# Performance work log

Measured on AMD Instinct MI355X. Metric: run time of the kernel, lower is better.

The kernel has to match this reference:

```python
import jax, jax.numpy as jnp
import numpy as np

B, S, E, H, L, A, OBS = 4, 1024, 512, 8, 4, 8, 128
D_HEAD = E // H
EPS = 1e-6
DECAY_SCALING = 1.0


def rmsnorm(x, scale):
    return x * jax.lax.rsqrt(jnp.mean(x * x, -1, keepdims=True) + EPS) * scale


def swiglu_ffn(x, w_gate, w_lin, w_out):
    return (jax.nn.silu(x @ w_gate) * (x @ w_lin)) @ w_out


def retention(x, h, logk, w_q, w_k, w_v, w_g, w_o, gns, gnb, ts, seg):
    # x:[B,S,E]  h:[B,H,d,d]  ts/seg:[B,S] int  logk:[H]
    q = (x @ w_q).reshape(B, S, H, D_HEAD).transpose(0, 2, 1, 3)
    k = (x @ w_k).reshape(B, S, H, D_HEAD).transpose(0, 2, 1, 3) / jnp.sqrt(jnp.asarray(D_HEAD, x.dtype))
    v = (x @ w_v).reshape(B, S, H, D_HEAD).transpose(0, 2, 1, 3)
    dt = (ts[:, :, None] - ts[:, None, :]).astype(x.dtype)            # [B,S,S]
    mask = (dt >= 0) & (seg[:, :, None] == seg[:, None, :])           # timestep-causal, same episode
    dt = jnp.where(mask, dt, 0.0)
    Dm = jnp.where(mask[:, None], jnp.exp(dt[:, None] * logk[None, :, None, None]), 0.0)  # [B,H,S,S]
    scores = jnp.einsum('bhnd,bhmd->bhnm', q, k) * Dm
    inner = jnp.einsum('bhnm,bhme->bhne', scores, v)
    tsf = ts.astype(x.dtype)
    fresh = (seg == 0).astype(x.dtype)                                # prev-chunk state only valid pre-done
    xi = jnp.exp((tsf + 1.0)[:, None, :] * logk[None, :, None]) * fresh[:, None, :]  # [B,H,S]
    cross = jnp.einsum('bhn,bhnd,bhde->bhne', xi, q, h)
    ret = inner + cross                                               # [B,H,S,d]
    # chunk-final recurrent state
    tmax = tsf[:, -1]
    eta = jnp.exp((tmax[:, None] - tsf)[:, None, :] * logk[None, :, None])
    eta = eta * (seg == seg[:, -1:]).astype(x.dtype)[:, None, :]
    keep = (seg[:, -1] == 0).astype(x.dtype)
    h_decay = jnp.exp((tmax + 1.0)[:, None] * logk[None, :]) * keep[:, None]  # [B,H]
    h_new = h * h_decay[..., None, None] + jnp.einsum('bhm,bhmd,bhme->bhde', eta, k, v)
    # per-head group norm (num_groups = n_head)
    y = ret.transpose(0, 2, 1, 3)                                     # [B,S,H,d]
    mu = jnp.mean(y, -1, keepdims=True)
    var = jnp.mean((y - mu) ** 2, -1, keepdims=True)
    y = ((y - mu) * jax.lax.rsqrt(var + EPS)).reshape(B, S, E) * gns + gnb
    out = (jax.nn.silu(x @ w_g) * y) @ w_o
    return out, h_new


def forward(obs, hstate, dones, timestep_id, ln_enc_scale, w_enc, ln_shared,
            wq, wk, wv, wg, wo, gn_scale, gn_bias, ln1_s, ln2_s,
            sw_gate, sw_lin, sw_out, head_w1, head_b1, head_ln, head_w2, head_b2):
    kappas = (1.0 - jnp.exp(jnp.linspace(jnp.log(1.0 / 32.0), jnp.log(1.0 / 512.0), H))) * DECAY_SCALING
    logk = jnp.log(kappas).astype(obs.dtype)
    seg = jnp.cumsum(dones, axis=-1)
    x = jax.nn.gelu(rmsnorm(obs, ln_enc_scale) @ w_enc)               # obs encoder
    new_h = jnp.zeros_like(hstate)
    for i in range(L):
        xin = rmsnorm(x, ln_shared)
        ret, hn = retention(xin, hstate[:, :, i], logk, wq[i], wk[i], wv[i], wg[i], wo[i],
                            gn_scale[i], gn_bias[i], timestep_id, seg)
        x1 = rmsnorm(xin + ret, ln1_s[i])
        x = rmsnorm(x1 + swiglu_ffn(x1, sw_gate[i], sw_lin[i], sw_out[i]), ln2_s[i])
        new_h = new_h.at[:, :, i].set(hn)
    z = jax.nn.gelu(x @ head_w1 + head_b1)
    v_loc = rmsnorm(z, head_ln) @ head_w2 + head_b2
    return v_loc, x, new_h


def setup_inputs() -> dict:
    key = jax.random.key(0)
    ks = jax.random.split(key, 16)
    sc = 0.02
    f = jnp.float32
    return {
        'obs': jax.random.normal(ks[0], (B, S, OBS), f),
        'hstate': jax.random.normal(ks[1], (B, H, L, D_HEAD, D_HEAD), f) * 0.1,
        'dones': (jax.random.uniform(ks[2], (B, S)) < 0.01).astype(jnp.int32),
        'timestep_id': jnp.broadcast_to(jnp.repeat(jnp.arange(S // A, dtype=jnp.int32), A)[None], (B, S)),
        'ln_enc_scale': jnp.ones((OBS,), f),
        'w_enc': jax.random.normal(ks[3], (OBS, E), f) * sc,
        'ln_shared': jnp.ones((E,), f),
        'wq': jax.random.normal(ks[4], (L, E, E), f) * sc,
        'wk': jax.random.normal(ks[5], (L, E, E), f) * sc,
        'wv': jax.random.normal(ks[6], (L, E, E), f) * sc,
        'wg': jax.random.normal(ks[7], (L, E, E), f) * sc,
        'wo': jax.random.normal(ks[8], (L, E, E), f) * sc,
        'gn_scale': jnp.ones((L, E), f),
        'gn_bias': jnp.zeros((L, E), f),
        'ln1_s': jnp.ones((L, E), f),
        'ln2_s': jnp.ones((L, E), f),
        'sw_gate': jax.random.normal(ks[9], (L, E, E), f) * sc,
        'sw_lin': jax.random.normal(ks[10], (L, E, E), f) * sc,
        'sw_out': jax.random.normal(ks[11], (L, E, E), f) * sc,
        'head_w1': jax.random.normal(ks[12], (E, E), f) * sc,
        'head_b1': jnp.zeros((E,), f),
        'head_ln': jnp.ones((E,), f),
        'head_w2': jax.random.normal(ks[13], (E, 1), f) * 0.01,
        'head_b2': jnp.zeros((1,), f),
    }


def reference(obs, hstate, dones, timestep_id, ln_enc_scale, w_enc, ln_shared,
              wq, wk, wv, wg, wo, gn_scale, gn_bias, ln1_s, ln2_s,
              sw_gate, sw_lin, sw_out, head_w1, head_b1, head_ln, head_w2, head_b2):
    return forward(obs, hstate, dones, timestep_id, ln_enc_scale, w_enc, ln_shared,
                   wq, wk, wv, wg, wo, gn_scale, gn_bias, ln1_s, ln2_s,
                   sw_gate, sw_lin, sw_out, head_w1, head_b1, head_ln, head_w2, head_b2)
```

## Files before the change

### kernel.cpp

```cpp
#include <hip/hip_runtime.h>
#include <math.h>

#define BN 4
#define SN 1024
#define EN 512
#define HN 8
#define LN 4
#define DN 64
#define OBSN 128
#define NR (BN*SN)
#define NB (NR*EN)
#define EPSF 1e-6f

typedef __attribute__((ext_vector_type(8))) short short8v;
typedef __attribute__((ext_vector_type(4))) float f32x4;
typedef unsigned short u16;

__device__ __forceinline__ float logk_of(int h){
    const float start = -3.4657359027997265f;
    const float step  = -0.3960841031771117f;
    return logf(1.0f - expf(start + step*(float)h));
}
__device__ __forceinline__ float geluf(float x){
    float x3 = x*x*x;
    return 0.5f*x*(1.0f + tanhf(0.7978845608028654f*(x + 0.044715f*x3)));
}
__device__ __forceinline__ float siluf(float x){
    return x / (1.0f + expf(-x));
}
__device__ __forceinline__ u16 f2bf(float x){
    union { float f; unsigned u; } v; v.f = x;
    unsigned r = v.u + 0x7FFFu + ((v.u >> 16) & 1u);
    return (u16)(r >> 16);
}
__device__ __forceinline__ float bf2f(u16 x){
    union { unsigned u; float f; } v; v.u = ((unsigned)x)<<16;
    return v.f;
}
__device__ __forceinline__ void load_lds16(const void* g, void* l){
    __builtin_amdgcn_global_load_lds((const __attribute__((address_space(1))) void*)g,
                                     (__attribute__((address_space(3))) void*)l, 16, 0, 0);
}
__device__ __forceinline__ int swz(int r, int bo){ return r*128 + (bo ^ ((r&7)<<4)); }

__device__ __forceinline__ float rx_of(int mode, const float* ssA, const float* ssB, int row){
    float rn = rsqrtf(ssA[row]*(1.f/512.f) + EPSF);
    if (mode==0) return rn;
    return rn*rsqrtf(rn*rn*ssB[row]*(1.f/512.f) + EPSF);
}

__global__ void seg_kernel(const int* __restrict__ dones, int* __restrict__ seg){
    __shared__ int sm[SN];
    int b = blockIdx.x, t = threadIdx.x;
    sm[t] = dones[b*SN + t];
    __syncthreads();
    for (int off=1; off<SN; off<<=1){
        int v = (t>=off) ? sm[t-off] : 0;
        __syncthreads();
        sm[t] += v;
        __syncthreads();
    }
    seg[b*SN + t] = sm[t];
}

__global__ void lnvq_kernel(const float* __restrict__ lnsh, const float* __restrict__ ln2,
                            float* __restrict__ lnvq){
    int k = threadIdx.x;
    #pragma unroll
    for (int l=0;l<LN;l++)
        lnvq[l*EN + k] = lnsh[k] * (l ? ln2[(l-1)*EN + k] : 1.f);
}

__global__ void wconv8_kernel(const float* w0, const float* w1, const float* w2,
                              const float* w3, const float* w4, const float* w5,
                              const float* w6, const float* w7,
                              const float* __restrict__ lnvq, const float* __restrict__ ln1,
                              u16* __restrict__ dst){
    __shared__ u16 tile[32][33];
    int z = blockIdx.z;
    int type = z>>2, layer = z&3;
    const float* srcs[8] = {w0,w1,w2,w3,w4,w5,w6,w7};
    const float* s = srcs[type] + (size_t)layer*EN*EN;
    u16* d = dst + ((size_t)type*LN + layer)*EN*EN;
    int k0 = blockIdx.y*32, m0 = blockIdx.x*32;
    int tx = threadIdx.x, ty = threadIdx.y;
    #pragma unroll
    for (int i=0;i<32;i+=8){
        int k = k0+ty+i;
        float sc = 1.f;
        if (type<4) sc = lnvq[layer*EN + k];
        else if (type==5 || type==6) sc = ln1[layer*EN + k];
        tile[tx][ty+i] = f2bf(s[(size_t)k*EN + m0+tx]*sc);
    }
    __syncthreads();
    #pragma unroll
    for (int i=0;i<32;i+=8)
        d[(size_t)(m0+ty+i)*EN + k0+tx] = tile[ty+i][tx];
}
__global__ void wconv_kernel(const float* __restrict__ src, u16* __restrict__ dst,
                             int K, int M){
    __shared__ u16 tile[32][33];
    int k0 = blockIdx.y*32, m0 = blockIdx.x*32;
    int tx = threadIdx.x, ty = threadIdx.y;
    #pragma unroll
    for (int i=0;i<32;i+=8)
        tile[tx][ty+i] = f2bf(src[(size_t)(k0+ty+i)*M + m0+tx]);
    __syncthreads();
    #pragma unroll
    for (int i=0;i<32;i+=8)
        dst[(size_t)(m0+ty+i)*K + k0+tx] = tile[ty+i][tx];
}

__global__ void rmsobs_kernel(const float* __restrict__ A, const float* __restrict__ scale,
                              u16* __restrict__ Ob){
    int row  = blockIdx.x*4 + (threadIdx.x>>6);
    int lane = threadIdx.x & 63;
    const float* a = A + (size_t)row*OBSN;
    float v0 = a[lane], v1 = a[lane+64];
    float ss = v0*v0 + v1*v1;
    #pragma unroll
    for (int off=32; off>0; off>>=1) ss += __shfl_xor(ss, off, 64);
    float rs = rsqrtf(ss*(1.0f/OBSN) + EPSF);
    Ob[(size_t)row*OBSN + lane]      = f2bf(v0*rs*scale[lane]);
    Ob[(size_t)row*OBSN + lane + 64] = f2bf(v1*rs*scale[lane+64]);
}

__device__ __forceinline__ void stage_tile(const u16* __restrict__ G, size_t rowBase,
                                           int K, int k0, u16* dst, int t){
    #pragma unroll
    for (int i=0;i<2;i++){
        int o = i*4096 + t*16;
        int grow = o>>7, gcolb = o&127;
        load_lds16(G + (rowBase+grow)*K + k0 + (gcolb>>1), (char*)dst + o);
    }
}
__device__ __forceinline__ void mma_tile(const u16* As, const u16* Bs, f32x4 acc[2][2],
                                         int wr, int wc, int lane){
    #pragma unroll
    for (int kk=0; kk<64; kk+=32){
        int kb = kk + (lane>>4)*8;
        short8v a[2], b[2];
        #pragma unroll
        for (int m=0;m<2;m++)
            a[m] = *(const short8v*)((const char*)As + (wr*32+m*16+(lane&15))*128 + kb*2);
        #pragma unroll
        for (int n=0;n<2;n++)
            b[n] = *(const short8v*)((const char*)Bs + (wc*32+n*16+(lane&15))*128 + kb*2);
        #pragma unroll
        for (int m=0;m<2;m++)
            #pragma unroll
            for (int n=0;n<2;n++)
                acc[m][n] = __builtin_amdgcn_mfma_f32_16x16x32_bf16(a[m], b[n], acc[m][n], 0,0,0);
    }
}
#define ZERO_ACC(acc) { _Pragma("unroll") for (int m=0;m<2;m++) _Pragma("unroll") for (int n=0;n<2;n++){ acc[m][n][0]=0.f;acc[m][n][1]=0.f;acc[m][n][2]=0.f;acc[m][n][3]=0.f; } }

__device__ __forceinline__ void ss_atomic(float v, float* __restrict__ ss, int row, int lane){
    #pragma unroll
    for (int off=1; off<16; off<<=1) v += __shfl_xor(v, off, 16);
    if ((lane&15)==0) atomicAdd(&ss[row], v);
}

__global__ __launch_bounds__(256) void gemm_enc(
    const u16* __restrict__ A, const u16* __restrict__ Wt,
    float* __restrict__ Xf, u16* __restrict__ Xb, float* __restrict__ ssA)
{
    __shared__ u16 As[2][64*64];
    __shared__ u16 Bs[2][64*64];
    int t = threadIdx.x;
    int row0 = blockIdx.y*64, col0 = blockIdx.x*64;
    int w = t>>6, lane = t&63;
    int wr = w>>1, wc = w&1;
    f32x4 acc[2][2];
    ZERO_ACC(acc);
    stage_tile(A, (size_t)row0, OBSN, 0, As[0], t);
    stage_tile(Wt, (size_t)col0, OBSN, 0, Bs[0], t);
    __syncthreads();
    for (int ti=0; ti<OBSN/64; ++ti){
        int cur = ti&1;
        if (ti+1 < OBSN/64){
            stage_tile(A, (size_t)row0, OBSN, (ti+1)*64, As[cur^1], t);
            stage_tile(Wt, (size_t)col0, OBSN, (ti+1)*64, Bs[cur^1], t);
        }
        mma_tile(As[cur], Bs[cur], acc, wr, wc, lane);
        __syncthreads();
    }
    #pragma unroll
    for (int m=0;m<2;m++){
        #pragma unroll
        for (int j=0;j<4;j++){
            int row = row0 + wr*32 + m*16 + (lane>>4)*4 + j;
            float sv = 0.f;
            #pragma unroll
            for (int n=0;n<2;n++){
                int col = col0 + wc*32 + n*16 + (lane&15);
                float x = geluf(acc[m][n][j]);
                Xf[(size_t)row*EN + col] = x;
                Xb[(size_t)row*EN + col] = f2bf(x);
                sv += x*x;
            }
            ss_atomic(sv, ssA, row, lane);
        }
    }
}

__global__ __launch_bounds__(256) void gemm_qkvg(
    const u16* __restrict__ A,
    const u16* __restrict__ WQ, const u16* __restrict__ WK,
    const u16* __restrict__ WV, const u16* __restrict__ WG,
    const float* __restrict__ ssA, const float* __restrict__ ssB, int mode,
    u16* __restrict__ Qbb, u16* __restrict__ Kbb,
    u16* __restrict__ VtT, u16* __restrict__ KtT, float* __restrict__ Gb)
{
    __shared__ u16 As[2][64*64];
    __shared__ u16 Bs[2][4][64*64];
    int t = threadIdx.x;
    int row0 = blockIdx.y*64, col0 = blockIdx.x*64;
    int w = t>>6, lane = t&63;
    int wr = w>>1, wc = w&1;
    f32x4 accQ[2][2], accK[2][2], accV[2][2], accG[2][2];
    ZERO_ACC(accQ); ZERO_ACC(accK); ZERO_ACC(accV); ZERO_ACC(accG);
    const u16* Ws[4] = {WQ, WK, WV, WG};

    stage_tile(A, (size_t)row0, EN, 0, As[0], t);
    #pragma unroll
    for (int wt=0; wt<4; wt++) stage_tile(Ws[wt], (size_t)col0, EN, 0, Bs[0][wt], t);
    __syncthreads();
    for (int ti=0; ti<EN/64; ++ti){
        int cur = ti&1;
        if (ti+1 < EN/64){
            stage_tile(A, (size_t)row0, EN, (ti+1)*64, As[cur^1], t);
            #pragma unroll
            for (int wt=0; wt<4; wt++)
                stage_tile(Ws[wt], (size_t)col0, EN, (ti+1)*64, Bs[cur^1][wt], t);
        }
        mma_tile(As[cur], Bs[cur][0], accQ, wr, wc, lane);
        mma_tile(As[cur], Bs[cur][1], accK, wr, wc, lane);
        mma_tile(As[cur], Bs[cur][2], accV, wr, wc, lane);
        mma_tile(As[cur], Bs[cur][3], accG, wr, wc, lane);
        __syncthreads();
    }
    float rxv[2][4];
    #pragma unroll
    for (int m=0;m<2;m++)
        #pragma unroll
        for (int j=0;j<4;j++)
            rxv[m][j] = rx_of(mode, ssA, ssB, row0 + wr*32 + m*16 + (lane>>4)*4 + j);
    #pragma unroll
    for (int m=0;m<2;m++){
        #pragma unroll
        for (int n=0;n<2;n++){
            int col = col0 + wc*32 + n*16 + (lane&15);
            int rbase = row0 + wr*32 + m*16 + (lane>>4)*4;
            ushort4 pkV, pkK;
            #pragma unroll
            for (int j=0;j<4;j++){
                float rx = rxv[m][j];
                size_t idx = (size_t)(rbase+j)*EN + col;
                Qbb[idx] = f2bf(rx*accQ[m][n][j]);
                float kx = rx*accK[m][n][j]*0.125f;
                Kbb[idx] = f2bf(kx);
                ((u16*)&pkK)[j] = f2bf(kx);
                ((u16*)&pkV)[j] = f2bf(rx*accV[m][n][j]);
                Gb[idx] = siluf(rx*accG[m][n][j]);
            }
            int bb = rbase>>10;
            int s0 = rbase&1023;
            *(ushort4*)(VtT + ((size_t)bb*EN + col)*SN + s0) = pkV;
            *(ushort4*)(KtT + ((size_t)bb*EN + col)*SN + s0) = pkK;
        }
    }
}

__global__ __launch_bounds__(256) void gemm_wo(
    const u16* __restrict__ A, const u16* __restrict__ Wt,
    const float* __restrict__ Xf, const float* __restrict__ lnv,
    const float* __restrict__ ssA, const float* __restrict__ ssB, int mode,
    float* __restrict__ Y1f, u16* __restrict__ Y1b, float* __restrict__ ss1)
{
    __shared__ u16 As[2][64*64];
    __shared__ u16 Bs[2][64*64];
    int t = threadIdx.x;
    int row0 = blockIdx.y*64, col0 = blockIdx.x*64;
    int w = t>>6, lane = t&63;
    int wr = w>>1, wc = w&1;
    f32x4 acc[2][2];
    ZERO_ACC(acc);
    stage_tile(A, (size_t)row0, EN, 0, As[0], t);
    stage_tile(Wt, (size_t)col0, EN, 0, Bs[0], t);
    __syncthreads();
    for (int ti=0; ti<EN/64; ++ti){
        int cur = ti&1;
        if (ti+1 < EN/64){
            stage_tile(A, (size_t)row0, EN, (ti+1)*64, As[cur^1], t);
            stage_tile(Wt, (size_t)col0, EN, (ti+1)*64, Bs[cur^1], t);
        }
        mma_tile(As[cur], Bs[cur], acc, wr, wc, lane);
        __syncthreads();
    }
    #pragma unroll
    for (int m=0;m<2;m++){
        #pragma unroll
        for (int j=0;j<4;j++){
            int row = row0 + wr*32 + m*16 + (lane>>4)*4 + j;
            float rx = rx_of(mode, ssA, ssB, row);
            float sv = 0.f;
            #pragma unroll
            for (int n=0;n<2;n++){
                int col = col0 + wc*32 + n*16 + (lane&15);
                size_t idx = (size_t)row*EN + col;
                float x = acc[m][n][j] + rx*lnv[col]*Xf[idx];
                Y1f[idx] = x;
                Y1b[idx] = f2bf(x);
                sv += x*x;
            }
            ss_atomic(sv, ss1, row, lane);
        }
    }
}

__global__ __launch_bounds__(256) void gemm_swpair(
    const u16* __restrict__ A,
    const u16* __restrict__ WGt, const u16* __restrict__ WLt,
    const float* __restrict__ ss1, u16* __restrict__ Out)
{
    __shared__ u16 As[2][64*64];
    __shared__ u16 Bg[2][64*64];
    __shared__ u16 Bl[2][64*64];
    int t = threadIdx.x;
    int row0 = blockIdx.y*64, col0 = blockIdx.x*64;
    int w = t>>6, lane = t&63;
    int wr = w>>1, wc = w&1;
    f32x4 accG[2][2], accL[2][2];
    ZERO_ACC(accG); ZERO_ACC(accL);
    stage_tile(A, (size_t)row0, EN, 0, As[0], t);
    stage_tile(WGt, (size_t)col0, EN, 0, Bg[0], t);
    stage_tile(WLt, (size_t)col0, EN, 0, Bl[0], t);
    __syncthreads();
    for (int ti=0; ti<EN/64; ++ti){
        int cur = ti&1;
        if (ti+1 < EN/64){
            stage_tile(A, (size_t)row0, EN, (ti+1)*64, As[cur^1], t);
            stage_tile(WGt, (size_t)col0, EN, (ti+1)*64, Bg[cur^1], t);
            stage_tile(WLt, (size_t)col0, EN, (ti+1)*64, Bl[cur^1], t);
        }
        mma_tile(As[cur], Bg[cur], accG, wr, wc, lane);
        mma_tile(As[cur], Bl[cur], accL, wr, wc, lane);
        __syncthreads();
    }
    #pragma unroll
    for (int m=0;m<2;m++){
        #pragma unroll
        for (int n=0;n<2;n++){
            int col = col0 + wc*32 + n*16 + (lane&15);
            int rbase = row0 + wr*32 + m*16 + (lane>>4)*4;
            #pragma unroll
            for (int j=0;j<4;j++){
                float r1 = rx_of(0, ss1, nullptr, rbase+j);
                float x = siluf(r1*accG[m][n][j]) * (r1*accL[m][n][j]);
                Out[(size_t)(rbase+j)*EN + col] = f2bf(x);
            }
        }
    }
}

__global__ __launch_bounds__(256) void gemm_swo(
    const u16* __restrict__ A, const u16* __restrict__ Wt,
    const float* __restrict__ Y1f, const float* __restrict__ ln1,
    const float* __restrict__ ss1, const float* __restrict__ ln2,
    float* __restrict__ Xf, u16* __restrict__ Xb,
    float* __restrict__ ssA, float* __restrict__ ssB)
{
    __shared__ u16 As[2][64*64];
    __shared__ u16 Bs[2][64*64];
    int t = threadIdx.x;
    int row0 = blockIdx.y*64, col0 = blockIdx.x*64;
    int w = t>>6, lane = t&63;
    int wr = w>>1, wc = w&1;
    f32x4 acc[2][2];
    ZERO_ACC(acc);
    stage_tile(A, (size_t)row0, EN, 0, As[0], t);
    stage_tile(Wt, (size_t)col0, EN, 0, Bs[0], t);
    __syncthreads();
    for (int ti=0; ti<EN/64; ++ti){
        int cur = ti&1;
        if (ti+1 < EN/64){
            stage_tile(A, (size_t)row0, EN, (ti+1)*64, As[cur^1], t);
            stage_tile(Wt, (size_t)col0, EN, (ti+1)*64, Bs[cur^1], t);
        }
        mma_tile(As[cur], Bs[cur], acc, wr, wc, lane);
        __syncthreads();
    }
    #pragma unroll
    for (int m=0;m<2;m++){
        #pragma unroll
        for (int j=0;j<4;j++){
            int row = row0 + wr*32 + m*16 + (lane>>4)*4 + j;
            float r1 = rx_of(0, ss1, nullptr, row);
            float svA = 0.f, svB = 0.f;
            #pragma unroll
            for (int n=0;n<2;n++){
                int col = col0 + wc*32 + n*16 + (lane&15);
                size_t idx = (size_t)row*EN + col;
                float x = acc[m][n][j] + r1*ln1[col]*Y1f[idx];
                Xf[idx] = x;
                Xb[idx] = f2bf(x);
                svA += x*x;
                float xw = x*ln2[col];
                svB += xw*xw;
            }
            ss_atomic(svA, ssA, row, lane);
            ss_atomic(svB, ssB, row, lane);
        }
    }
}

__global__ __launch_bounds__(256) void gemm_head(
    const u16* __restrict__ A, const u16* __restrict__ Wt,
    const float* __restrict__ bias, float* __restrict__ C)
{
    __shared__ u16 As[2][64*64];
    __shared__ u16 Bs[2][64*64];
    int t = threadIdx.x;
    int row0 = blockIdx.y*64, col0 = blockIdx.x*64;
    int w = t>>6, lane = t&63;
    int wr = w>>1, wc = w&1;
    f32x4 acc[2][2];
    ZERO_ACC(acc);
    stage_tile(A, (size_t)row0, EN, 0, As[0], t);
    stage_tile(Wt, (size_t)col0, EN, 0, Bs[0], t);
    __syncthreads();
    for (int ti=0; ti<EN/64; ++ti){
        int cur = ti&1;
        if (ti+1 < EN/64){
            stage_tile(A, (size_t)row0, EN, (ti+1)*64, As[cur^1], t);
            stage_tile(Wt, (size_t)col0, EN, (ti+1)*64, Bs[cur^1], t);
        }
        mma_tile(As[cur], Bs[cur], acc, wr, wc, lane);
        __syncthreads();
    }
    #pragma unroll
    for (int m=0;m<2;m++){
        #pragma unroll
        for (int n=0;n<2;n++){
            int col = col0 + wc*32 + n*16 + (lane&15);
            int rbase = row0 + wr*32 + m*16 + (lane>>4)*4;
            #pragma unroll
            for (int j=0;j<4;j++)
                C[(size_t)(rbase+j)*EN + col] = geluf(acc[m][n][j] + bias[col]);
        }
    }
}

__global__ __launch_bounds__(256) void retention_mfma(
    const u16* __restrict__ Qbb, const u16* __restrict__ Kbb,
    const u16* __restrict__ VtT, const u16* __restrict__ KtT,
    const float* __restrict__ hstate, const int* __restrict__ tsid, const int* __restrict__ seg,
    const float* __restrict__ gns, const float* __restrict__ gnb,
    const float* __restrict__ Gb, u16* __restrict__ Out,
    float* __restrict__ Hout, int layer)
{
    int bh = blockIdx.y; int b = bh>>3; int h = bh&7;
    int t = threadIdx.x, lane = t&63, w = t>>6;
    __shared__ u16 Qs[64*64];
    __shared__ u16 Ks[64*64];
    __shared__ u16 Vts[64*64];
    __shared__ u16 Ps[64*64];
    __shared__ float tsq_s[64], eq_s[64], xi_s[64];
    __shared__ int   segq_s[64];
    __shared__ float tsm_s[64], em_s[64];
    __shared__ int   segm_s[64];
    float lk = logk_of(h);

    if (blockIdx.x == 0){
        float tmax = (float)tsid[b*SN + SN-1];
        int segl = seg[b*SN + SN-1];
        float* eta = (float*)Qs;
        #pragma unroll
        for (int i=0;i<4;i++){
            int m = t + i*256;
            float tsm = (float)tsid[b*SN+m];
            eta[m] = (seg[b*SN+m]==segl) ? expf((tmax - tsm)*lk) : 0.f;
        }
        f32x4 eacc[4];
        #pragma unroll
        for (int en=0;en<4;en++){ eacc[en][0]=0.f; eacc[en][1]=0.f; eacc[en][2]=0.f; eacc[en][3]=0.f; }
        for (int mt=0; mt<16; ++mt){
            int m0 = mt*64;
            __syncthreads();
            #pragma unroll
            for (int i=0;i<2;i++){
                int c = t + i*256; int r = c>>3, cb = (c&7)*16;
                int mb = m0 + (cb>>1);
                size_t g = ((size_t)(b*EN) + h*DN + r)*SN + mb;
                short8v kt = *(const short8v*)(KtT + g);
                short8v vt = *(const short8v*)(VtT + g);
                short8v ks;
                #pragma unroll
                for (int j=0;j<8;j++) ks[j] = (short)f2bf(bf2f((u16)kt[j]) * eta[mb+j]);
                *(short8v*)((char*)Ks  + swz(r,cb)) = ks;
                *(short8v*)((char*)Vts + swz(r,cb)) = vt;
            }
            __syncthreads();
            short8v a0 = *(short8v*)((char*)Ks + swz(w*16+(lane&15), (lane>>4)*16));
            short8v a1 = *(short8v*)((char*)Ks + swz(w*16+(lane&15), 64+(lane>>4)*16));
            __builtin_amdgcn_s_setprio(1);
            #pragma unroll
            for (int en=0;en<4;en++){
                short8v b0 = *(short8v*)((char*)Vts + swz(en*16+(lane&15), (lane>>4)*16));
                short8v b1 = *(short8v*)((char*)Vts + swz(en*16+(lane&15), 64+(lane>>4)*16));
                eacc[en] = __builtin_amdgcn_mfma_f32_16x16x32_bf16(a0, b0, eacc[en], 0,0,0);
                eacc[en] = __builtin_amdgcn_mfma_f32_16x16x32_bf16(a1, b1, eacc[en], 0,0,0);
            }
            __builtin_amdgcn_s_setprio(0);
        }
        float hd = (segl==0) ? expf((tmax+1.0f)*lk) : 0.f;
        const float* h0 = hstate + ((size_t)bh*LN + layer)*4096;
        float* ho = Hout + ((size_t)bh*LN + layer)*4096;
        #pragma unroll
        for (int en=0;en<4;en++){
            int e = en*16 + (lane&15);
            #pragma unroll
            for (int j=0;j<4;j++){
                int d = w*16 + (lane>>4)*4 + j;
                ho[d*64 + e] = h0[d*64 + e]*hd + eacc[en][j];
            }
        }
        return;
    }

    int tile = 16 - (int)blockIdx.x;
    int n0 = tile*64;

    #pragma unroll
    for (int i=0;i<2;i++){
        int c = t + i*256; int r = c>>3, cb = (c&7)*16;
        short8v qv = *(const short8v*)(Qbb + (size_t)(b*SN + n0 + r)*EN + h*DN + (cb>>1));
        *(short8v*)((char*)Qs + swz(r,cb)) = qv;
    }
    const float* h0 = hstate + ((size_t)bh*LN + layer)*4096;
    #pragma unroll
    for (int i=0;i<4;i++){
        int idx = t + i*256; int d = idx>>4, e0 = (idx&15)*4;
        float4 hv = *(const float4*)(h0 + d*64 + e0);
        *(u16*)((char*)Ps + swz(e0+0, 2*d)) = f2bf(hv.x);
        *(u16*)((char*)Ps + swz(e0+1, 2*d)) = f2bf(hv.y);
        *(u16*)((char*)Ps + swz(e0+2, 2*d)) = f2bf(hv.z);
        *(u16*)((char*)Ps + swz(e0+3, 2*d)) = f2bf(hv.w);
    }
    if (t<64){
        float tq = (float)tsid[b*SN+n0+t];
        int sg = seg[b*SN+n0+t];
        tsq_s[t]=tq; segq_s[t]=sg;
        eq_s[t]=expf(tq*lk);
        xi_s[t]=(sg==0)?expf((tq+1.f)*lk):0.f;
    }
    short8v kr0, kr1, vr0, vr1;
    {
        int c0 = t, c1 = t+256;
        int r0=c0>>3, cb0=(c0&7)*16, r1=c1>>3, cb1=(c1&7)*16;
        kr0 = *(const short8v*)(Kbb + (size_t)(b*SN+r0)*EN + h*DN + (cb0>>1));
        kr1 = *(const short8v*)(Kbb + (size_t)(b*SN+r1)*EN + h*DN + (cb1>>1));
        vr0 = *(const short8v*)(VtT + ((size_t)(b*EN)+h*DN+r0)*SN + (cb0>>1));
        vr1 = *(const short8v*)(VtT + ((size_t)(b*EN)+h*DN+r1)*SN + (cb1>>1));
    }
    __syncthreads();

    int qlj = w*16 + ((lane>>4)<<2);
    float tsq_r[4], eq_r[4], xi_r[4]; int sgq_r[4];
    #pragma unroll
    for (int j=0;j<4;j++){
        tsq_r[j]=tsq_s[qlj+j]; eq_r[j]=eq_s[qlj+j];
        xi_r[j]=xi_s[qlj+j];  sgq_r[j]=segq_s[qlj+j];
    }
    short8v aq0 = *(short8v*)((char*)Qs + swz(w*16+(lane&15), (lane>>4)*16));
    short8v aq1 = *(short8v*)((char*)Qs + swz(w*16+(lane&15), 64 + (lane>>4)*16));

    f32x4 oacc[4];
    {
        f32x4 cacc[4];
        #pragma unroll
        for (int en=0;en<4;en++){ cacc[en][0]=0.f; cacc[en][1]=0.f; cacc[en][2]=0.f; cacc[en][3]=0.f; }
        #pragma unroll
        for (int en=0;en<4;en++){
            short8v b0 = *(short8v*)((char*)Ps + swz(en*16+(lane&15), (lane>>4)*16));
            short8v b1 = *(short8v*)((char*)Ps + swz(en*16+(lane&15), 64+(lane>>4)*16));
            cacc[en] = __builtin_amdgcn_mfma_f32_16x16x32_bf16(aq0, b0, cacc[en], 0,0,0);
            cacc[en] = __builtin_amdgcn_mfma_f32_16x16x32_bf16(aq1, b1, cacc[en], 0,0,0);
        }
        #pragma unroll
        for (int en=0;en<4;en++)
            #pragma unroll
            for (int j=0;j<4;j++) oacc[en][j] = cacc[en][j]*xi_r[j];
    }

    for (int mt=0; mt<=tile; ++mt){
        int m0 = mt*64;
        __syncthreads();
        {
            int c0 = t, c1 = t+256;
            int r0=c0>>3, cb0=(c0&7)*16, r1=c1>>3, cb1=(c1&7)*16;
            *(short8v*)((char*)Ks  + swz(r0,cb0)) = kr0;
            *(short8v*)((char*)Ks  + swz(r1,cb1)) = kr1;
            *(short8v*)((char*)Vts + swz(r0,cb0)) = vr0;
            *(short8v*)((char*)Vts + swz(r1,cb1)) = vr1;
        }
        if (t<64){
            float tm = (float)tsid[b*SN+m0+t];
            tsm_s[t]=tm; segm_s[t]=seg[b*SN+m0+t]; em_s[t]=expf(-tm*lk);
        }
        if (mt < tile){
            int m1 = m0 + 64;
            int c0 = t, c1 = t+256;
            int r0=c0>>3, cb0=(c0&7)*16, r1=c1>>3, cb1=(c1&7)*16;
            kr0 = *(const short8v*)(Kbb + (size_t)(b*SN+m1+r0)*EN + h*DN + (cb0>>1));
            kr1 = *(const short8v*)(Kbb + (size_t)(b*SN+m1+r1)*EN + h*DN + (cb1>>1));
            vr0 = *(const short8v*)(VtT + ((size_t)(b*EN)+h*DN+r0)*SN + m1 + (cb0>>1));
            vr1 = *(const short8v*)(VtT + ((size_t)(b*EN)+h*DN+r1)*SN + m1 + (cb1>>1));
        }
        __syncthreads();
        f32x4 sacc[4];
        #pragma unroll
        for (int mn=0;mn<4;mn++){ sacc[mn][0]=0.f; sacc[mn][1]=0.f; sacc[mn][2]=0.f; sacc[mn][3]=0.f; }
        __builtin_amdgcn_s_setprio(1);
        #pragma unroll
        for (int mn=0;mn<4;mn++){
            short8v b0 = *(short8v*)((char*)Ks + swz(mn*16+(lane&15), (lane>>4)*16));
            short8v b1 = *(short8v*)((char*)Ks + swz(mn*16+(lane&15), 64+(lane>>4)*16));
            sacc[mn] = __builtin_amdgcn_mfma_f32_16x16x32_bf16(aq0, b0, sacc[mn], 0,0,0);
            sacc[mn] = __builtin_amdgcn_mfma_f32_16x16x32_bf16(aq1, b1, sacc[mn], 0,0,0);
        }
        __builtin_amdgcn_s_setprio(0);
        #pragma unroll
        for (int mn=0;mn<4;mn++){
            int m = mn*16 + (lane&15);
            float tm = tsm_s[m]; float em = em_s[m]; int sgm = segm_s[m];
            #pragma unroll
            for (int j=0;j<4;j++){
                float p = (tsq_r[j]>=tm && sgq_r[j]==sgm) ? sacc[mn][j]*eq_r[j]*em : 0.f;
                *(u16*)((char*)Ps + swz(qlj+j, 2*m)) = f2bf(p);
            }
        }
        short8v ap0 = *(short8v*)((char*)Ps + swz(w*16+(lane&15), (lane>>4)*16));
        short8v ap1 = *(short8v*)((char*)Ps + swz(w*16+(lane&15), 64+(lane>>4)*16));
        __builtin_amdgcn_s_setprio(1);
        #pragma unroll
        for (int dn=0;dn<4;dn++){
            short8v b0 = *(short8v*)((char*)Vts + swz(dn*16+(lane&15), (lane>>4)*16));
            short8v b1 = *(short8v*)((char*)Vts + swz(dn*16+(lane&15), 64+(lane>>4)*16));
            oacc[dn] = __builtin_amdgcn_mfma_f32_16x16x32_bf16(ap0, b0, oacc[dn], 0,0,0);
            oacc[dn] = __builtin_amdgcn_mfma_f32_16x16x32_bf16(ap1, b1, oacc[dn], 0,0,0);
        }
        __builtin_amdgcn_s_setprio(0);
    }

    float mu[4], rs[4];
    #pragma unroll
    for (int j=0;j<4;j++){
        float s = oacc[0][j]+oacc[1][j]+oacc[2][j]+oacc[3][j];
        #pragma unroll
        for (int off=1; off<16; off<<=1) s += __shfl_xor(s, off, 64);
        mu[j] = s*(1.0f/64.0f);
        float d0=oacc[0][j]-mu[j], d1=oacc[1][j]-mu[j], d2=oacc[2][j]-mu[j], d3=oacc[3][j]-mu[j];
        float q2 = d0*d0+d1*d1+d2*d2+d3*d3;
        #pragma unroll
        for (int off=1; off<16; off<<=1) q2 += __shfl_xor(q2, off, 64);
        rs[j] = rsqrtf(q2*(1.0f/64.0f) + EPSF);
    }
    #pragma unroll
    for (int dn=0;dn<4;dn++){
        int e = h*DN + dn*16 + (lane&15);
        float gs = gns[e], gb = gnb[e];
        #pragma unroll
        for (int j=0;j<4;j++){
            size_t row = (size_t)(b*SN + n0 + qlj + j);
            float y = (oacc[dn][j]-mu[j])*rs[j]*gs + gb;
            Out[row*EN + e] = f2bf(y * Gb[row*EN + e]);
        }
    }
}

__global__ void xout_kernel(const float* __restrict__ Xf, const float* __restrict__ ssA,
                            const float* __restrict__ ln23,
                            float* __restrict__ out_x, u16* __restrict__ Xb){
    int row  = blockIdx.x*4 + (threadIdx.x>>6);
    int lane = threadIdx.x & 63;
    float rn = rsqrtf(ssA[row]*(1.f/512.f) + EPSF);
    #pragma unroll
    for (int i=0;i<8;i++){
        int col = lane + i*64;
        float x = rn * Xf[(size_t)row*EN + col] * ln23[col];
        out_x[(size_t)row*EN + col] = x;
        Xb[(size_t)row*EN + col] = f2bf(x);
    }
}

__global__ void vloc_kernel(const float* __restrict__ Z, const float* __restrict__ hln,
                            const float* __restrict__ w2, const float* __restrict__ b2,
                            float* __restrict__ out){
    int row  = blockIdx.x*4 + (threadIdx.x>>6);
    int lane = threadIdx.x & 63;
    const float* z = Z + (size_t)row*EN;
    float ss = 0.f, dot = 0.f;
    #pragma unroll
    for (int i=0;i<8;i++){
        int col = lane + i*64;
        float zv = z[col];
        ss += zv*zv;
        dot += zv*hln[col]*w2[col];
    }
    #pragma unroll
    for (int off=32; off>0; off>>=1){
        ss += __shfl_xor(ss, off, 64);
        dot += __shfl_xor(dot, off, 64);
    }
    if (lane==0) out[row] = rsqrtf(ss*(1.f/512.f)+EPSF)*dot + b2[0];
}

extern "C" void kernel_launch(void* const* d_in, const int* in_sizes, int n_in,
                              void* d_out, int out_size, void* d_ws, size_t ws_size,
                              hipStream_t stream){
    const float* obs       = (const float*)d_in[0];
    const float* hstate    = (const float*)d_in[1];
    const int*   dones     = (const int*)  d_in[2];
    const int*   tsid      = (const int*)  d_in[3];
    const float* ln_enc    = (const float*)d_in[4];
    const float* w_enc     = (const float*)d_in[5];
    const float* ln_shared = (const float*)d_in[6];
    const float* wq        = (const float*)d_in[7];
    const float* wk        = (const float*)d_in[8];
    const float* wv        = (const float*)d_in[9];
    const float* wg        = (const float*)d_in[10];
    const float* wo        = (const float*)d_in[11];
    const float* gns       = (const float*)d_in[12];
    const float* gnb       = (const float*)d_in[13];
    const float* ln1       = (const float*)d_in[14];
    const float* ln2       = (const float*)d_in[15];
    const float* swg       = (const float*)d_in[16];
    const float* swl       = (const float*)d_in[17];
    const float* swo       = (const float*)d_in[18];
    const float* hw1       = (const float*)d_in[19];
    const float* hb1       = (const float*)d_in[20];
    const float* hln       = (const float*)d_in[21];
    const float* hw2       = (const float*)d_in[22];
    const float* hb2       = (const float*)d_in[23];

    float* out_v = (float*)d_out;
    float* out_x = out_v + NR;
    float* out_h = out_x + (size_t)NR*EN;

    float* ws    = (float*)d_ws;
    float* Xf    = ws + 0*(size_t)NB;
    float* Qs32  = ws + 1*(size_t)NB;
    float* Y1f   = ws + 2*(size_t)NB;
    float* Gb    = ws + 3*(size_t)NB;
    float* Zb    = ws + 4*(size_t)NB;
    int*   seg   = (int*)(ws + 5*(size_t)NB);
    u16* wtb  = (u16*)(seg + NR);
    const size_t WEm = (size_t)EN*EN;
    u16* wqT   = wtb;
    u16* woT   = wtb + 4*4*WEm;
    u16* wencT = wtb + 8*4*WEm;
    u16* w1T   = wencT + (size_t)EN*OBSN;
    u16* Xb    = w1T + WEm;
    u16* S2b   = Xb  + (size_t)NB;
    u16* Y1b   = S2b + (size_t)NB;
    u16* encb  = Y1b + (size_t)NB;
    u16* Qbb   = encb + (size_t)NR*OBSN;
    u16* Kbb   = Qbb + (size_t)NB;
    u16* VtT   = (u16*)Qs32;
    u16* KtT   = VtT + (size_t)NB;
    float* ssBase = (float*)(Kbb + (size_t)NB);
    float* ssA   = ssBase;
    float* ssB   = ssA + 5*NR;
    float* ss1   = ssB + 5*NR;
    float* lnvq  = ss1 + 4*NR;

    hipMemsetAsync(ssBase, 0, (5*NR + 5*NR + 4*NR)*sizeof(float), stream);

    seg_kernel<<<BN, SN, 0, stream>>>(dones, seg);
    lnvq_kernel<<<1, EN, 0, stream>>>(ln_shared, ln2, lnvq);
    {
        dim3 tb(32,8,1);
        wconv8_kernel<<<dim3(16,16,32), tb, 0, stream>>>(wq,wk,wv,wg,wo,swg,swl,swo, lnvq, ln1, wtb);
        wconv_kernel<<<dim3(16,4,1),  tb, 0, stream>>>(w_enc, wencT, OBSN, EN);
        wconv_kernel<<<dim3(16,16,1), tb, 0, stream>>>(hw1,   w1T,   EN, EN);
    }

    rmsobs_kernel<<<NR/4, 256, 0, stream>>>(obs, ln_enc, encb);
    gemm_enc<<<dim3(8,64), 256, 0, stream>>>(encb, wencT, Xf, Xb, ssA);

    for (int l=0; l<LN; ++l){
        int mode = (l==0) ? 0 : 1;
        const float* sA = ssA + l*NR;
        const float* sB = ssB + l*NR;
        float* s1 = ss1 + l*NR;
        gemm_qkvg<<<dim3(8,64), 256, 0, stream>>>(Xb,
            wtb + (0*LN+l)*WEm, wtb + (1*LN+l)*WEm, wtb + (2*LN+l)*WEm, wtb + (3*LN+l)*WEm,
            sA, sB, mode, Qbb, Kbb, VtT, KtT, Gb);
        retention_mfma<<<dim3(17, BN*HN), 256, 0, stream>>>(
            Qbb, Kbb, VtT, KtT, hstate, tsid, seg, gns + l*EN, gnb + l*EN,
            Gb, S2b, out_h, l);
        gemm_wo<<<dim3(8,64), 256, 0, stream>>>(S2b, wtb + (4*LN+l)*WEm,
            Xf, lnvq + l*EN, sA, sB, mode, Y1f, Y1b, s1);
        gemm_swpair<<<dim3(8,64), 256, 0, stream>>>(Y1b,
            wtb + (5*LN+l)*WEm, wtb + (6*LN+l)*WEm, s1, S2b);
        gemm_swo<<<dim3(8,64), 256, 0, stream>>>(S2b, wtb + (7*LN+l)*WEm,
            Y1f, ln1 + l*EN, s1, ln2 + l*EN,
            Xf, Xb, ssA + (l+1)*NR, ssB + (l+1)*NR);
    }

    xout_kernel<<<NR/4, 256, 0, stream>>>(Xf, ssA + LN*NR, ln2 + 3*EN, out_x, Xb);
    gemm_head<<<dim3(8,64), 256, 0, stream>>>(Xb, w1T, hb1, Zb);
    vloc_kernel<<<NR/4, 256, 0, stream>>>(Zb, hln, hw2, hb2, out_v);
}
```

Measured before the change: 458.4 us.

## Factor retention decay into Q/K scaling and double-buffer retention tiles

The exponential decay exp((tq-tm)*logk) is split into per-row factors. exp(tq*logk) is folded into Q and exp(-tm*logk) into K inside the QKVG GEMM epilogue, so the retention inner loop only applies masks instead of computing exponentials per element. The cross-chunk and final-state terms are rescaled to match. The K/V tiles in both retention loops are double-buffered in shared memory so there is one barrier per iteration, and the QKVG GEMM is split across a z grid dimension of two (Q/K vs V/G) to cut LDS and registers per block. The cost is a numerical risk: storing exp-scaled Q and K in bf16 can reach large or small magnitudes when timesteps are large.

```diff
diff --git a/kernel.cpp b/kernel.cpp
--- a/kernel.cpp
+++ b/kernel.cpp
@@ -32,10 +32,6 @@
     union { float f; unsigned u; } v; v.f = x;
     unsigned r = v.u + 0x7FFFu + ((v.u >> 16) & 1u);
     return (u16)(r >> 16);
-}
-__device__ __forceinline__ float bf2f(u16 x){
-    union { unsigned u; float f; } v; v.u = ((unsigned)x)<<16;
-    return v.f;
 }
 __device__ __forceinline__ void load_lds16(const void* g, void* l){
     __builtin_amdgcn_global_load_lds((const __attribute__((address_space(1))) void*)g,
@@ -208,36 +204,36 @@
     const u16* __restrict__ A,
     const u16* __restrict__ WQ, const u16* __restrict__ WK,
     const u16* __restrict__ WV, const u16* __restrict__ WG,
+    const int* __restrict__ tsid,
     const float* __restrict__ ssA, const float* __restrict__ ssB, int mode,
     u16* __restrict__ Qbb, u16* __restrict__ Kbb,
     u16* __restrict__ VtT, u16* __restrict__ KtT, float* __restrict__ Gb)
 {
     __shared__ u16 As[2][64*64];
-    __shared__ u16 Bs[2][4][64*64];
+    __shared__ u16 B0[2][64*64];
+    __shared__ u16 B1[2][64*64];
     int t = threadIdx.x;
+    int z = blockIdx.z;
     int row0 = blockIdx.y*64, col0 = blockIdx.x*64;
     int w = t>>6, lane = t&63;
     int wr = w>>1, wc = w&1;
-    f32x4 accQ[2][2], accK[2][2], accV[2][2], accG[2][2];
-    ZERO_ACC(accQ); ZERO_ACC(accK); ZERO_ACC(accV); ZERO_ACC(accG);
-    const u16* Ws[4] = {WQ, WK, WV, WG};
-
-    stage_tile(A, (size_t)row0, EN, 0, As[0], t);
-    #pragma unroll
-    for (int wt=0; wt<4; wt++) stage_tile(Ws[wt], (size_t)col0, EN, 0, Bs[0][wt], t);
+    const u16* Wa = z ? WV : WQ;
+    const u16* Wb = z ? WG : WK;
+    f32x4 acc0[2][2], acc1[2][2];
+    ZERO_ACC(acc0); ZERO_ACC(acc1);
+    stage_tile(A,  (size_t)row0, EN, 0, As[0], t);
+    stage_tile(Wa, (size_t)col0, EN, 0, B0[0], t);
+    stage_tile(Wb, (size_t)col0, EN, 0, B1[0], t);
     __syncthreads();
     for (int ti=0; ti<EN/64; ++ti){
         int cur = ti&1;
         if (ti+1 < EN/64){
-            stage_tile(A, (size_t)row0, EN, (ti+1)*64, As[cur^1], t);
-            #pragma unroll
-            for (int wt=0; wt<4; wt++)
-                stage_tile(Ws[wt], (size_t)col0, EN, (ti+1)*64, Bs[cur^1][wt], t);
-        }
-        mma_tile(As[cur], Bs[cur][0], accQ, wr, wc, lane);
-        mma_tile(As[cur], Bs[cur][1], accK, wr, wc, lane);
-        mma_tile(As[cur], Bs[cur][2], accV, wr, wc, lane);
-        mma_tile(As[cur], Bs[cur][3], accG, wr, wc, lane);
+            stage_tile(A,  (size_t)row0, EN, (ti+1)*64, As[cur^1], t);
+            stage_tile(Wa, (size_t)col0, EN, (ti+1)*64, B0[cur^1], t);
+            stage_tile(Wb, (size_t)col0, EN, (ti+1)*64, B1[cur^1], t);
+        }
+        mma_tile(As[cur], B0[cur], acc0, wr, wc, lane);
+        mma_tile(As[cur], B1[cur], acc1, wr, wc, lane);
         __syncthreads();
     }
     float rxv[2][4];
@@ -246,28 +242,57 @@
         #pragma unroll
         for (int j=0;j<4;j++)
             rxv[m][j] = rx_of(mode, ssA, ssB, row0 + wr*32 + m*16 + (lane>>4)*4 + j);
-    #pragma unroll
-    for (int m=0;m<2;m++){
-        #pragma unroll
-        for (int n=0;n<2;n++){
-            int col = col0 + wc*32 + n*16 + (lane&15);
-            int rbase = row0 + wr*32 + m*16 + (lane>>4)*4;
-            ushort4 pkV, pkK;
+
+    if (z==0){
+        float lk = logk_of(blockIdx.x);
+        float eqv[2][4], emv[2][4];
+        #pragma unroll
+        for (int m=0;m<2;m++)
             #pragma unroll
             for (int j=0;j<4;j++){
-                float rx = rxv[m][j];
-                size_t idx = (size_t)(rbase+j)*EN + col;
-                Qbb[idx] = f2bf(rx*accQ[m][n][j]);
-                float kx = rx*accK[m][n][j]*0.125f;
-                Kbb[idx] = f2bf(kx);
-                ((u16*)&pkK)[j] = f2bf(kx);
-                ((u16*)&pkV)[j] = f2bf(rx*accV[m][n][j]);
-                Gb[idx] = siluf(rx*accG[m][n][j]);
-            }
-            int bb = rbase>>10;
-            int s0 = rbase&1023;
-            *(ushort4*)(VtT + ((size_t)bb*EN + col)*SN + s0) = pkV;
-            *(ushort4*)(KtT + ((size_t)bb*EN + col)*SN + s0) = pkK;
+                int row = row0 + wr*32 + m*16 + (lane>>4)*4 + j;
+                float tq = (float)tsid[row];
+                eqv[m][j] = expf(tq*lk);
+                emv[m][j] = expf(-tq*lk);
+            }
+        #pragma unroll
+        for (int m=0;m<2;m++){
+            #pragma unroll
+            for (int n=0;n<2;n++){
+                int col = col0 + wc*32 + n*16 + (lane&15);
+                int rbase = row0 + wr*32 + m*16 + (lane>>4)*4;
+                ushort4 pkK;
+                #pragma unroll
+                for (int j=0;j<4;j++){
+                    size_t idx = (size_t)(rbase+j)*EN + col;
+                    Qbb[idx] = f2bf(rxv[m][j]*eqv[m][j]*acc0[m][n][j]);
+                    float kx = rxv[m][j]*emv[m][j]*0.125f*acc1[m][n][j];
+                    Kbb[idx] = f2bf(kx);
+                    ((u16*)&pkK)[j] = f2bf(kx);
+                }
+                int bb = rbase>>10;
+                int s0 = rbase&1023;
+                *(ushort4*)(KtT + ((size_t)bb*EN + col)*SN + s0) = pkK;
+            }
+        }
+    } else {
+        #pragma unroll
+        for (int m=0;m<2;m++){
+            #pragma unroll
+            for (int n=0;n<2;n++){
+                int col = col0 + wc*32 + n*16 + (lane&15);
+                int rbase = row0 + wr*32 + m*16 + (lane>>4)*4;
+                ushort4 pkV;
+                #pragma unroll
+                for (int j=0;j<4;j++){
+                    size_t idx = (size_t)(rbase+j)*EN + col;
+                    ((u16*)&pkV)[j] = f2bf(rxv[m][j]*acc0[m][n][j]);
+                    Gb[idx] = siluf(rxv[m][j]*acc1[m][n][j]);
+                }
+                int bb = rbase>>10;
+                int s0 = rbase&1023;
+                *(ushort4*)(VtT + ((size_t)bb*EN + col)*SN + s0) = pkV;
+            }
         }
     }
 }
@@ -463,57 +488,80 @@
     int bh = blockIdx.y; int b = bh>>3; int h = bh&7;
     int t = threadIdx.x, lane = t&63, w = t>>6;
     __shared__ u16 Qs[64*64];
-    __shared__ u16 Ks[64*64];
-    __shared__ u16 Vts[64*64];
+    __shared__ u16 Ks[2][64*64];
+    __shared__ u16 Vts[2][64*64];
     __shared__ u16 Ps[64*64];
-    __shared__ float tsq_s[64], eq_s[64], xi_s[64];
+    __shared__ float tsq_s[64];
     __shared__ int   segq_s[64];
-    __shared__ float tsm_s[64], em_s[64];
-    __shared__ int   segm_s[64];
+    __shared__ float tsm_s[2][64];
+    __shared__ int   segm_s[2][64];
     float lk = logk_of(h);
+
+    int c0i = t, c1i = t+256;
+    int r0=c0i>>3, cb0=(c0i&7)*16, r1=c1i>>3, cb1=(c1i&7)*16;
 
     if (blockIdx.x == 0){
         float tmax = (float)tsid[b*SN + SN-1];
         int segl = seg[b*SN + SN-1];
-        float* eta = (float*)Qs;
+        u16* m16 = Qs;
         #pragma unroll
         for (int i=0;i<4;i++){
             int m = t + i*256;
-            float tsm = (float)tsid[b*SN+m];
-            eta[m] = (seg[b*SN+m]==segl) ? expf((tmax - tsm)*lk) : 0.f;
-        }
+            m16[m] = (seg[b*SN+m]==segl) ? (u16)0xFFFFu : (u16)0;
+        }
+        __syncthreads();
+        size_t g0 = ((size_t)(b*EN) + h*DN + r0)*SN + (cb0>>1);
+        size_t g1 = ((size_t)(b*EN) + h*DN + r1)*SN + (cb1>>1);
+        short8v kr0, kr1, vr0, vr1;
+        {
+            kr0 = *(const short8v*)(KtT + g0);
+            vr0 = *(const short8v*)(VtT + g0);
+            kr1 = *(const short8v*)(KtT + g1);
+            vr1 = *(const short8v*)(VtT + g1);
+            short8v mv0 = *(const short8v*)(m16 + (cb0>>1));
+            short8v mv1 = *(const short8v*)(m16 + (cb1>>1));
+            kr0 &= mv0; kr1 &= mv1;
+            *(short8v*)((char*)Ks[0]  + swz(r0,cb0)) = kr0;
+            *(short8v*)((char*)Ks[0]  + swz(r1,cb1)) = kr1;
+            *(short8v*)((char*)Vts[0] + swz(r0,cb0)) = vr0;
+            *(short8v*)((char*)Vts[0] + swz(r1,cb1)) = vr1;
+        }
+        __syncthreads();
         f32x4 eacc[4];
         #pragma unroll
         for (int en=0;en<4;en++){ eacc[en][0]=0.f; eacc[en][1]=0.f; eacc[en][2]=0.f; eacc[en][3]=0.f; }
         for (int mt=0; mt<16; ++mt){
-            int m0 = mt*64;
-            __syncthreads();
-            #pragma unroll
-            for (int i=0;i<2;i++){
-                int c = t + i*256; int r = c>>3, cb = (c&7)*16;
-                int mb = m0 + (cb>>1);
-                size_t g = ((size_t)(b*EN) + h*DN + r)*SN + mb;
-                short8v kt = *(const short8v*)(KtT + g);
-                short8v vt = *(const short8v*)(VtT + g);
-                short8v ks;
-                #pragma unroll
-                for (int j=0;j<8;j++) ks[j] = (short)f2bf(bf2f((u16)kt[j]) * eta[mb+j]);
-                *(short8v*)((char*)Ks  + swz(r,cb)) = ks;
-                *(short8v*)((char*)Vts + swz(r,cb)) = vt;
-            }
-            __syncthreads();
-            short8v a0 = *(short8v*)((char*)Ks + swz(w*16+(lane&15), (lane>>4)*16));
-            short8v a1 = *(short8v*)((char*)Ks + swz(w*16+(lane&15), 64+(lane>>4)*16));
+            int cur = mt&1;
+            if (mt<15){
+                int m1 = (mt+1)*64;
+                kr0 = *(const short8v*)(KtT + g0 + m1);
+                vr0 = *(const short8v*)(VtT + g0 + m1);
+                kr1 = *(const short8v*)(KtT + g1 + m1);
+                vr1 = *(const short8v*)(VtT + g1 + m1);
+                short8v mv0 = *(const short8v*)(m16 + m1 + (cb0>>1));
+                short8v mv1 = *(const short8v*)(m16 + m1 + (cb1>>1));
+                kr0 &= mv0; kr1 &= mv1;
+            }
+            short8v a0 = *(short8v*)((char*)Ks[cur] + swz(w*16+(lane&15), (lane>>4)*16));
+            short8v a1 = *(short8v*)((char*)Ks[cur] + swz(w*16+(lane&15), 64+(lane>>4)*16));
             __builtin_amdgcn_s_setprio(1);
             #pragma unroll
             for (int en=0;en<4;en++){
-                short8v b0 = *(short8v*)((char*)Vts + swz(en*16+(lane&15), (lane>>4)*16));
-                short8v b1 = *(short8v*)((char*)Vts + swz(en*16+(lane&15), 64+(lane>>4)*16));
+                short8v b0 = *(short8v*)((char*)Vts[cur] + swz(en*16+(lane&15), (lane>>4)*16));
+                short8v b1 = *(short8v*)((char*)Vts[cur] + swz(en*16+(lane&15), 64+(lane>>4)*16));
                 eacc[en] = __builtin_amdgcn_mfma_f32_16x16x32_bf16(a0, b0, eacc[en], 0,0,0);
                 eacc[en] = __builtin_amdgcn_mfma_f32_16x16x32_bf16(a1, b1, eacc[en], 0,0,0);
             }
             __builtin_amdgcn_s_setprio(0);
-        }
+            if (mt<15){
+                *(short8v*)((char*)Ks[cur^1]  + swz(r0,cb0)) = kr0;
+                *(short8v*)((char*)Ks[cur^1]  + swz(r1,cb1)) = kr1;
+                *(short8v*)((char*)Vts[cur^1] + swz(r0,cb0)) = vr0;
+                *(short8v*)((char*)Vts[cur^1] + swz(r1,cb1)) = vr1;
+                __syncthreads();
+            }
+        }
+        float cfac = expf(tmax*lk);
         float hd = (segl==0) ? expf((tmax+1.0f)*lk) : 0.f;
         const float* h0 = hstate + ((size_t)bh*LN + layer)*4096;
         float* ho = Hout + ((size_t)bh*LN + layer)*4096;
@@ -523,7 +571,7 @@
             #pragma unroll
             for (int j=0;j<4;j++){
                 int d = w*16 + (lane>>4)*4 + j;
-                ho[d*64 + e] = h0[d*64 + e]*hd + eacc[en][j];
+                ho[d*64 + e] = h0[d*64 + e]*hd + cfac*eacc[en][j];
             }
         }
         return;
@@ -549,29 +597,32 @@
         *(u16*)((char*)Ps + swz(e0+3, 2*d)) = f2bf(hv.w);
     }
     if (t<64){
-        float tq = (float)tsid[b*SN+n0+t];
-        int sg = seg[b*SN+n0+t];
-        tsq_s[t]=tq; segq_s[t]=sg;
-        eq_s[t]=expf(tq*lk);
-        xi_s[t]=(sg==0)?expf((tq+1.f)*lk):0.f;
+        tsq_s[t] = (float)tsid[b*SN+n0+t];
+        segq_s[t] = seg[b*SN+n0+t];
+        tsm_s[0][t] = (float)tsid[b*SN+t];
+        segm_s[0][t] = seg[b*SN+t];
     }
     short8v kr0, kr1, vr0, vr1;
     {
-        int c0 = t, c1 = t+256;
-        int r0=c0>>3, cb0=(c0&7)*16, r1=c1>>3, cb1=(c1&7)*16;
         kr0 = *(const short8v*)(Kbb + (size_t)(b*SN+r0)*EN + h*DN + (cb0>>1));
         kr1 = *(const short8v*)(Kbb + (size_t)(b*SN+r1)*EN + h*DN + (cb1>>1));
         vr0 = *(const short8v*)(VtT + ((size_t)(b*EN)+h*DN+r0)*SN + (cb0>>1));
         vr1 = *(const short8v*)(VtT + ((size_t)(b*EN)+h*DN+r1)*SN + (cb1>>1));
+        *(short8v*)((char*)Ks[0]  + swz(r0,cb0)) = kr0;
+        *(short8v*)((char*)Ks[0]  + swz(r1,cb1)) = kr1;
+        *(short8v*)((char*)Vts[0] + swz(r0,cb0)) = vr0;
+        *(short8v*)((char*)Vts[0] + swz(r1,cb1)) = vr1;
     }
     __syncthreads();
 
     int qlj = w*16 + ((lane>>4)<<2);
-    float tsq_r[4], eq_r[4], xi_r[4]; int sgq_r[4];
+    float tsq_r[4]; int sgq_r[4]; float xr[4];
+    float elk = expf(lk);
     #pragma unroll
     for (int j=0;j<4;j++){
-        tsq_r[j]=tsq_s[qlj+j]; eq_r[j]=eq_s[qlj+j];
-        xi_r[j]=xi_s[qlj+j];  sgq_r[j]=segq_s[qlj+j];
+        tsq_r[j]=tsq_s[qlj+j];
+        sgq_r[j]=segq_s[qlj+j];
+        xr[j] = (sgq_r[j]==0) ? elk : 0.f;
     }
     short8v aq0 = *(short8v*)((char*)Qs + swz(w*16+(lane&15), (lane>>4)*16));
     short8v aq1 = *(short8v*)((char*)Qs + swz(w*16+(lane&15), 64 + (lane>>4)*16));
@@ -591,54 +642,53 @@
         #pragma unroll
         for (int en=0;en<4;en++)
             #pragma unroll
-            for (int j=0;j<4;j++) oacc[en][j] = cacc[en][j]*xi_r[j];
-    }
+            for (int j=0;j<4;j++) oacc[en][j] = cacc[en][j]*xr[j];
+    }
+    __syncthreads();
 
     for (int mt=0; mt<=tile; ++mt){
-        int m0 = mt*64;
-        __syncthreads();
-        {
-            int c0 = t, c1 = t+256;
-            int r0=c0>>3, cb0=(c0&7)*16, r1=c1>>3, cb1=(c1&7)*16;
-            *(short8v*)((char*)Ks  + swz(r0,cb0)) = kr0;
-            *(short8v*)((char*)Ks  + swz(r1,cb1)) = kr1;
-            *(short8v*)((char*)Vts + swz(r0,cb0)) = vr0;
-            *(short8v*)((char*)Vts + swz(r1,cb1)) = vr1;
-        }
-        if (t<64){
-            float tm = (float)tsid[b*SN+m0+t];
-            tsm_s[t]=tm; segm_s[t]=seg[b*SN+m0+t]; em_s[t]=expf(-tm*lk);
-        }
-        if (mt < tile){
-            int m1 = m0 + 64;
-            int c0 = t, c1 = t+256;
-            int r0=c0>>3, cb0=(c0&7)*16, r1=c1>>3, cb1=(c1&7)*16;
+        int cur = mt&1;
+        if (mt<tile){
+            int m1 = (mt+1)*64;
             kr0 = *(const short8v*)(Kbb + (size_t)(b*SN+m1+r0)*EN + h*DN + (cb0>>1));
             kr1 = *(const short8v*)(Kbb + (size_t)(b*SN+m1+r1)*EN + h*DN + (cb1>>1));
             vr0 = *(const short8v*)(VtT + ((size_t)(b*EN)+h*DN+r0)*SN + m1 + (cb0>>1));
             vr1 = *(const short8v*)(VtT + ((size_t)(b*EN)+h*DN+r1)*SN + m1 + (cb1>>1));
         }
-        __syncthreads();
         f32x4 sacc[4];
         #pragma unroll
         for (int mn=0;mn<4;mn++){ sacc[mn][0]=0.f; sacc[mn][1]=0.f; sacc[mn][2]=0.f; sacc[mn][3]=0.f; }
         __builtin_amdgcn_s_setprio(1);
         #pragma unroll
         for (int mn=0;mn<4;mn++){
-            short8v b0 = *(short8v*)((char*)Ks + swz(mn*16+(lane&15), (lane>>4)*16));
-            short8v b1 = *(short8v*)((char*)Ks + swz(mn*16+(lane&15), 64+(lane>>4)*16));
+            short8v b0 = *(short8v*)((char*)Ks[cur] + swz(mn*16+(lane&15), (lane>>4)*16));
+            short8v b1 = *(short8v*)((char*)Ks[cur] + swz(mn*16+(lane&15), 64+(lane>>4)*16));
             sacc[mn] = __builtin_amdgcn_mfma_f32_16x16x32_bf16(aq0, b0, sacc[mn], 0,0,0);
             sacc[mn] = __builtin_amdgcn_mfma_f32_16x16x32_bf16(aq1, b1, sacc[mn], 0,0,0);
         }
         __builtin_amdgcn_s_setprio(0);
-        #pragma unroll
-        for (int mn=0;mn<4;mn++){
-            int m = mn*16 + (lane&15);
-            float tm = tsm_s[m]; float em = em_s[m]; int sgm = segm_s[m];
-            #pragma unroll
-            for (int j=0;j<4;j++){
-                float p = (tsq_r[j]>=tm && sgq_r[j]==sgm) ? sacc[mn][j]*eq_r[j]*em : 0.f;
-                *(u16*)((char*)Ps + swz(qlj+j, 2*m)) = f2bf(p);
+        if (mt==tile){
+            #pragma unroll
+            for (int mn=0;mn<4;mn++){
+                int m = mn*16 + (lane&15);
+                int sgm = segm_s[cur][m];
+                float tm = tsm_s[cur][m];
+                #pragma unroll
+                for (int j=0;j<4;j++){
+                    float p = (tsq_r[j]>=tm && sgq_r[j]==sgm) ? sacc[mn][j] : 0.f;
+                    *(u16*)((char*)Ps + swz(qlj+j, 2*m)) = f2bf(p);
+                }
+            }
+        } else {
+            #pragma unroll
+            for (int mn=0;mn<4;mn++){
+                int m = mn*16 + (lane&15);
+                int sgm = segm_s[cur][m];
+                #pragma unroll
+                for (int j=0;j<4;j++){
+                    float p = (sgq_r[j]==sgm) ? sacc[mn][j] : 0.f;
+                    *(u16*)((char*)Ps + swz(qlj+j, 2*m)) = f2bf(p);
+                }
             }
         }
         short8v ap0 = *(short8v*)((char*)Ps + swz(w*16+(lane&15), (lane>>4)*16));
@@ -646,12 +696,24 @@
         __builtin_amdgcn_s_setprio(1);
         #pragma unroll
         for (int dn=0;dn<4;dn++){
-            short8v b0 = *(short8v*)((char*)Vts + swz(dn*16+(lane&15), (lane>>4)*16));
-            short8v b1 = *(short8v*)((char*)Vts + swz(dn*16+(lane&15), 64+(lane>>4)*16));
+            short8v b0 = *(short8v*)((char*)Vts[cur] + swz(dn*16+(lane&15), (lane>>4)*16));
+            short8v b1 = *(short8v*)((char*)Vts[cur] + swz(dn*16+(lane&15), 64+(lane>>4)*16));
             oacc[dn] = __builtin_amdgcn_mfma_f32_16x16x32_bf16(ap0, b0, oacc[dn], 0,0,0);
             oacc[dn] = __builtin_amdgcn_mfma_f32_16x16x32_bf16(ap1, b1, oacc[dn], 0,0,0);
         }
         __builtin_amdgcn_s_setprio(0);
+        if (mt<tile){
+            if (t<64){
+                int m1 = (mt+1)*64;
+                tsm_s[cur^1][t] = (float)tsid[b*SN+m1+t];
+                segm_s[cur^1][t] = seg[b*SN+m1+t];
+            }
+            *(short8v*)((char*)Ks[cur^1]  + swz(r0,cb0)) = kr0;
+            *(short8v*)((char*)Ks[cur^1]  + swz(r1,cb1)) = kr1;
+            *(short8v*)((char*)Vts[cur^1] + swz(r0,cb0)) = vr0;
+            *(short8v*)((char*)Vts[cur^1] + swz(r1,cb1)) = vr1;
+            __syncthreads();
+        }
     }
 
     float mu[4], rs[4];
@@ -758,8 +820,6 @@
     int*   seg   = (int*)(ws + 5*(size_t)NB);
     u16* wtb  = (u16*)(seg + NR);
     const size_t WEm = (size_t)EN*EN;
-    u16* wqT   = wtb;
-    u16* woT   = wtb + 4*4*WEm;
     u16* wencT = wtb + 8*4*WEm;
     u16* w1T   = wencT + (size_t)EN*OBSN;
     u16* Xb    = w1T + WEm;
@@ -795,9 +855,9 @@
         const float* sA = ssA + l*NR;
         const float* sB = ssB + l*NR;
         float* s1 = ss1 + l*NR;
-        gemm_qkvg<<<dim3(8,64), 256, 0, stream>>>(Xb,
+        gemm_qkvg<<<dim3(8,64,2), 256, 0, stream>>>(Xb,
             wtb + (0*LN+l)*WEm, wtb + (1*LN+l)*WEm, wtb + (2*LN+l)*WEm, wtb + (3*LN+l)*WEm,
-            sA, sB, mode, Qbb, Kbb, VtT, KtT, Gb);
+            tsid, sA, sB, mode, Qbb, Kbb, VtT, KtT, Gb);
         retention_mfma<<<dim3(17, BN*HN), 256, 0, stream>>>(
             Qbb, Kbb, VtT, KtT, hstate, tsid, seg, gns + l*EN, gnb + l*EN,
             Gb, S2b, out_h, l);
```

New measurement: 472.8 us. +3.1%, slower.
